# Kernel optimization log

Hardware: AMD Instinct MI355X
Metric: run time of the kernel (lower is better)

Reference implementation:

```python
import jax, jax.numpy as jnp
import numpy as np
from jax import lax

B, C, H, W = 16, 256, 64, 64  # inplanes=256, planes=2*inplanes=512


def ste_sign(x):
    # forward: sign(x); backward: clipped straight-through (|x|<=1)
    c = jnp.clip(x, -1.0, 1.0)
    return c + lax.stop_gradient(jnp.sign(x) - c)


def conv_ada(x, w, ka, kw):
    # 1-bit activations scaled by learnable scalar ka
    a_b = ste_sign(x) * ka
    # 1-bit weights with per-out-channel XNOR-style scale * learnable kw
    alpha = jnp.mean(jnp.abs(w), axis=(1, 2, 3), keepdims=True) * kw  # [O,1,1,1]
    w_b = ste_sign(w) * alpha
    return lax.conv_general_dilated(a_b, w_b, window_strides=(1, 1),
                                    padding=((1, 1), (1, 1)),
                                    dimension_numbers=('NCHW', 'OIHW', 'NCHW'))


def prelu(x, slope):
    s = slope.reshape(1, -1, 1, 1)
    return jnp.where(x >= 0, x, s * x)


def pixel_unshuffle2(x):
    b, c, h, w = x.shape
    x = x.reshape(b, c, h // 2, 2, w // 2, 2)
    x = x.transpose(0, 1, 3, 5, 2, 4)  # (b, c, r1, r2, h2, w2)
    return x.reshape(b, c * 4, h // 2, w // 2)


def setup_inputs() -> dict:
    key = jax.random.key(0)
    ks = jax.random.split(key, 8)
    inp = {
        'x': jax.random.normal(ks[0], (B, C, H, W), dtype=jnp.float32),
        'conv1_w': jax.random.normal(ks[1], (C, C, 3, 3), dtype=jnp.float32) * 0.05,
        'conv2_w': jax.random.normal(ks[2], (C // 2, C, 3, 3), dtype=jnp.float32) * 0.05,
        'bias1_': jnp.zeros((1, C, 1, 1), jnp.float32),
        'bias1': jnp.zeros((1, C, 1, 1), jnp.float32),
        'bias2': jnp.zeros((1, C, 1, 1), jnp.float32),
        'bias2_': jnp.zeros((1, C, 1, 1), jnp.float32),
        'bias3': jnp.zeros((1, C // 2, 1, 1), jnp.float32),
        'bias4': jnp.zeros((1, C // 2, 1, 1), jnp.float32),
        'ka1': jnp.asarray(1.0, jnp.float32),
        'kw1': jnp.asarray(0.2, jnp.float32),
        'ka2': jnp.asarray(1.0, jnp.float32),
        'kw2': jnp.asarray(0.2, jnp.float32),
        'prelu1_w': jnp.full((C,), 0.25, jnp.float32),
        'prelu2_w': jnp.full((C // 2,), 0.25, jnp.float32),
    }
    return inp


def reference(x, conv1_w, conv2_w, bias1_, bias1, bias2, bias2_, bias3, bias4,
              ka1, kw1, ka2, kw2, prelu1_w, prelu2_w):
    out = x + bias1_                      # move1_
    out = conv_ada(out, conv1_w, ka1, kw1)  # conv1
    xres = out + x                        # residual add
    # NOTE: in the original forward, move1/prelu1/move2 output is overwritten
    # (dead branch); kept here for faithfulness but it does not affect output.
    _dead = prelu(out + bias1, prelu1_w) + bias2
    out = xres + bias2_                   # move2_
    out = conv_ada(out, conv2_w, ka2, kw2)  # conv2 -> C//2 channels
    shortcut = xres[:, :xres.shape[1] // 2, :, :]
    out = out + shortcut
    out = out + bias3                     # move3
    out = prelu(out, prelu2_w)            # prelu2
    out = out + bias4                     # move4
    out = pixel_unshuffle2(out)           # -> [B, 2*C, H/2, W/2]
    return out
```

## Files before the change

### kernel.cpp

```cpp
#include <hip/hip_runtime.h>
#include <hip/hip_bf16.h>
#include <stdint.h>

#define B_   16
#define C_   256
#define H_   64
#define W_   64
#define PH   66
#define PW   66
#define K1   2304
#define NO1  256
#define NO2  128

typedef signed char i8;
typedef int   int32x4 __attribute__((ext_vector_type(4)));

__device__ __forceinline__ void gl_lds16(const void* src, void* dst) {
    __builtin_amdgcn_global_load_lds(
        (const __attribute__((address_space(1))) unsigned int*)src,
        (__attribute__((address_space(3))) unsigned int*)dst, 16, 0, 0);
}

__device__ __forceinline__ i8 sign_i8(float v) {
    return (v > 0.f) ? (i8)1 : ((v < 0.f) ? (i8)(-1) : (i8)0);
}

__global__ void halo_zero(i8* __restrict__ s1, i8* __restrict__ s2) {
    int t = blockIdx.x * blockDim.x + threadIdx.x;
    const int total = B_ * PH * PW * (C_ / 16);
    if (t >= total) return;
    int pix = t >> 4;
    int c16 = t & 15;
    int pw  = pix % PW;
    int ph  = (pix / PW) % PH;
    if (ph != 0 && ph != PH - 1 && pw != 0 && pw != PW - 1) return;
    int4 z = make_int4(0, 0, 0, 0);
    *(int4*)(s1 + (size_t)pix * C_ + c16 * 16) = z;
    *(int4*)(s2 + (size_t)pix * C_ + c16 * 16) = z;
}

__global__ void prep_s1(const float* __restrict__ x, const float* __restrict__ bias1_,
                        i8* __restrict__ s1) {
    __shared__ i8 tile[64][272];
    int b = blockIdx.x >> 6;
    int h = blockIdx.x & 63;
    int t = threadIdx.x;
    int w  = t & 63;
    int cq = t >> 6;
    for (int i = 0; i < 64; ++i) {
        int c = cq * 64 + i;
        float v = x[((size_t)(b * C_ + c) * H_ + h) * W_ + w] + bias1_[c];
        tile[w][c] = sign_i8(v);
    }
    __syncthreads();
    for (int i = 0; i < 4; ++i) {
        int idx = i * 256 + t;
        int w2  = idx >> 4;
        int cb  = (idx & 15) * 16;
        int4 v = *(const int4*)&tile[w2][cb];
        *(int4*)(s1 + ((size_t)(b * PH + h + 1) * PW + (w2 + 1)) * C_ + cb) = v;
    }
}

__global__ void prep_w(const float* __restrict__ w1, const float* __restrict__ w2,
                       const float* __restrict__ ka1, const float* __restrict__ kw1,
                       const float* __restrict__ ka2, const float* __restrict__ kw2,
                       i8* __restrict__ Bt1, i8* __restrict__ Bt2,
                       float* __restrict__ scale1, float* __restrict__ scale2) {
    int o = blockIdx.x;
    const float* w; i8* Bt; float* scale; float kk;
    if (o < NO1) { w = w1 + (size_t)o * K1;         Bt = Bt1 + (size_t)o * K1;         scale = scale1 + o;         kk = ka1[0] * kw1[0]; }
    else         { int oo = o - NO1;
                   w = w2 + (size_t)oo * K1;        Bt = Bt2 + (size_t)oo * K1;        scale = scale2 + oo;        kk = ka2[0] * kw2[0]; }
    int t = threadIdx.x;
    float s = 0.f;
    for (int e = t; e < K1; e += 256) {
        float v = w[e];
        s += fabsf(v);
        int c = e / 9, tap = e % 9;
        Bt[tap * 256 + c] = sign_i8(v);
    }
    for (int off = 32; off; off >>= 1) s += __shfl_down(s, off);
    __shared__ float red[4];
    if ((t & 63) == 0) red[t >> 6] = s;
    __syncthreads();
    if (t == 0) {
        float tot = red[0] + red[1] + red[2] + red[3];
        *scale = kk * tot * (1.0f / 2304.0f);
    }
}

template<int EPI>
__global__ __launch_bounds__(512)
void gemm_conv(const i8* __restrict__ Sin, const i8* __restrict__ Bt,
               const float* __restrict__ scale,
               const float* __restrict__ xaux,
               const float* __restrict__ biasA,
               const float* __restrict__ bias4,
               const float* __restrict__ slope,
               i8*   __restrict__ s2out,
               float* __restrict__ xres_out,
               float* __restrict__ dout)
{
    extern __shared__ char lds[];

    int t  = threadIdx.x;

    int wg    = blockIdx.x;
    int chunk = gridDim.x >> 3;
    int logical = (wg & 7) * chunk + (wg >> 3);
    int nb, mb;
    if (EPI == 1) { nb = logical & 1; mb = logical >> 1; }
    else          { nb = 0;           mb = logical; }
    int b  = mb >> 4;
    int h0 = (mb & 15) * 4;

    int r0  = t >> 3;
    int off = ((t & 7) * 16) ^ (((t >> 3) & 7) << 4);
    int lin = (t & 7) * 16;

    int l  = t & 63;
    int wv = t >> 6;
    int wr = wv >> 1;
    int wc = wv & 1;

    int32x4 acc[4][4];
#pragma unroll
    for (int mi = 0; mi < 4; ++mi)
#pragma unroll
        for (int ni = 0; ni < 4; ++ni) acc[mi][ni] = (int32x4){0, 0, 0, 0};

    auto stage = [&](int ks, char* buf) {
        char* As = buf;
        char* Bs = buf + 32768;
        int tap = ks >> 1;
        int c0  = (ks & 1) * 128;
        int dh  = tap / 3, dw = tap % 3;
#pragma unroll
        for (int i = 0; i < 4; ++i) {
            int r  = r0 + i * 64;
            int hh = r >> 6, ww = r & 63;
            const i8* ga = Sin + ((size_t)(b * PH + h0 + hh + dh) * PW + (ww + dw)) * C_ + c0 + off;
            gl_lds16(ga, As + r * 128 + lin);
        }
#pragma unroll
        for (int i = 0; i < 2; ++i) {
            int r = r0 + i * 64;
            int n = nb * 128 + r;
            const i8* gb = Bt + (size_t)n * K1 + tap * 256 + c0 + off;
            gl_lds16(gb, Bs + r * 128 + lin);
        }
    };

    auto compute = [&](const char* buf) {
        const char* As = buf;
        const char* Bs = buf + 32768;
        __builtin_amdgcn_s_setprio(1);
#pragma unroll
        for (int kk = 0; kk < 2; ++kk) {
            int kb = kk * 64 + ((l >> 4) * 16);
            int rx = (l & 7) << 4;
            int32x4 af[4], bf[4];
#pragma unroll
            for (int mi = 0; mi < 4; ++mi)
                af[mi] = *(const int32x4*)(As + (wr * 64 + mi * 16 + (l & 15)) * 128 + (kb ^ rx));
#pragma unroll
            for (int ni = 0; ni < 4; ++ni)
                bf[ni] = *(const int32x4*)(Bs + (wc * 64 + ni * 16 + (l & 15)) * 128 + (kb ^ rx));
#pragma unroll
            for (int mi = 0; mi < 4; ++mi)
#pragma unroll
                for (int ni = 0; ni < 4; ++ni)
                    acc[mi][ni] = __builtin_amdgcn_mfma_i32_16x16x64_i8(af[mi], bf[ni], acc[mi][ni], 0, 0, 0);
        }
        __builtin_amdgcn_s_setprio(0);
    };

    char* bc  = lds;
    char* bn  = lds + 49152;
    char* bn2 = lds + 98304;

    stage(0, bc);
    stage(1, bn);
    asm volatile("s_waitcnt vmcnt(6)" ::: "memory");
    __builtin_amdgcn_s_barrier();

    for (int ks = 0; ks < 18; ++ks) {
        if (ks < 16) stage(ks + 2, bn2);
        compute(bc);
        if (ks < 16)      asm volatile("s_waitcnt vmcnt(6)" ::: "memory");
        else if (ks == 16) asm volatile("s_waitcnt vmcnt(0)" ::: "memory");
        if (ks < 17) __builtin_amdgcn_s_barrier();
        char* tmp = bc; bc = bn; bn = bn2; bn2 = tmp;
    }

    int co = l & 15;
    int ro = l >> 4;
#pragma unroll
    for (int mi = 0; mi < 4; ++mi) {
#pragma unroll
        for (int ni = 0; ni < 4; ++ni) {
            int n_loc = wc * 64 + ni * 16 + co;
            int o = nb * 128 + n_loc;
            float sc = scale[o];
#pragma unroll
            for (int j = 0; j < 4; ++j) {
                int m_loc = wr * 64 + mi * 16 + ro * 4 + j;
                int h = h0 + (m_loc >> 6);
                int w = m_loc & 63;
                float v = (float)acc[mi][ni][j] * sc;
                if (EPI == 1) {
                    float xv = xaux[((size_t)(b * C_ + o) * H_ + h) * W_ + w];
                    float xr = v + xv;
                    float sv = xr + biasA[o];
                    s2out[((size_t)(b * PH + h + 1) * PW + (w + 1)) * C_ + o] = sign_i8(sv);
                    if (o < NO2)
                        xres_out[(((size_t)b * H_ + h) * W_ + w) * NO2 + o] = xr;
                } else {
                    float xr = xaux[(((size_t)b * H_ + h) * W_ + w) * NO2 + o];
                    float vv = v + xr + biasA[o];
                    vv = (vv >= 0.f) ? vv : vv * slope[o];
                    vv += bias4[o];
                    int p = h & 1, q = w & 1;
                    dout[(((size_t)b * 512 + (o * 4 + p * 2 + q)) * 32 + (h >> 1)) * 32 + (w >> 1)] = vv;
                }
            }
        }
    }
}

static const size_t SZ_S   = (size_t)B_ * PH * PW * C_;
static const size_t OFF_S1 = 0;
static const size_t OFF_S2 = OFF_S1 + SZ_S;
static const size_t OFF_B1 = OFF_S2 + SZ_S;
static const size_t OFF_B2 = OFF_B1 + (size_t)NO1 * K1;
static const size_t OFF_C1 = OFF_B2 + (size_t)NO2 * K1;
static const size_t OFF_C2 = OFF_C1 + 1024;
static const size_t OFF_XR = OFF_C2 + 512;

extern "C" void kernel_launch(void* const* d_in, const int* in_sizes, int n_in,
                              void* d_out, int out_size, void* d_ws, size_t ws_size,
                              hipStream_t stream) {
    (void)in_sizes; (void)n_in; (void)out_size; (void)ws_size;
    const float* x      = (const float*)d_in[0];
    const float* w1     = (const float*)d_in[1];
    const float* w2     = (const float*)d_in[2];
    const float* bias1_ = (const float*)d_in[3];
    const float* bias2_ = (const float*)d_in[6];
    const float* bias3  = (const float*)d_in[7];
    const float* bias4  = (const float*)d_in[8];
    const float* ka1    = (const float*)d_in[9];
    const float* kw1    = (const float*)d_in[10];
    const float* ka2    = (const float*)d_in[11];
    const float* kw2    = (const float*)d_in[12];
    const float* slope2 = (const float*)d_in[14];

    char* ws = (char*)d_ws;
    i8*    s1   = (i8*)(ws + OFF_S1);
    i8*    s2   = (i8*)(ws + OFF_S2);
    i8*    Bt1  = (i8*)(ws + OFF_B1);
    i8*    Bt2  = (i8*)(ws + OFF_B2);
    float* sc1  = (float*)(ws + OFF_C1);
    float* sc2  = (float*)(ws + OFF_C2);
    float* xres = (float*)(ws + OFF_XR);
    float* out  = (float*)d_out;

    {
        int total = B_ * PH * PW * (C_ / 16);
        hipLaunchKernelGGL(halo_zero, dim3((total + 255) / 256), dim3(256), 0, stream, s1, s2);
    }
    hipLaunchKernelGGL(prep_s1, dim3(B_ * H_), dim3(256), 0, stream, x, bias1_, s1);
    hipLaunchKernelGGL(prep_w, dim3(NO1 + NO2), dim3(256), 0, stream,
                       w1, w2, ka1, kw1, ka2, kw2, Bt1, Bt2, sc1, sc2);
    hipLaunchKernelGGL((gemm_conv<1>), dim3(512), dim3(512), 147456, stream,
                       s1, Bt1, sc1, x, bias2_, nullptr, nullptr, s2, xres, nullptr);
    hipLaunchKernelGGL((gemm_conv<2>), dim3(256), dim3(512), 147456, stream,
                       s2, Bt2, sc2, xres, bias3, bias4, slope2, nullptr, nullptr, out);
}
```

Measured before the change: 267.6 us.

## Load activation halo tile once into LDS and reuse across all nine taps

```diff
diff --git a/kernel.cpp b/kernel.cpp
--- a/kernel.cpp
+++ b/kernel.cpp
@@ -91,8 +91,9 @@
 }
 
 template<int EPI>
-__global__ __launch_bounds__(512)
-void gemm_conv(const i8* __restrict__ Sin, const i8* __restrict__ Bt,
+__device__ __forceinline__ void conv_body(
+               char* lds,
+               const i8* __restrict__ Sin, const i8* __restrict__ Bt,
                const float* __restrict__ scale,
                const float* __restrict__ xaux,
                const float* __restrict__ biasA,
@@ -102,7 +103,10 @@
                float* __restrict__ xres_out,
                float* __restrict__ dout)
 {
-    extern __shared__ char lds[];
+    char* Alds = lds;
+    char* Bs0  = lds + 101376;
+    char* Bs1  = Bs0 + 16384;
+    char* Bs2  = Bs1 + 16384;
 
     int t  = threadIdx.x;
 
@@ -115,83 +119,99 @@
     int b  = mb >> 4;
     int h0 = (mb & 15) * 4;
 
-    int r0  = t >> 3;
-    int off = ((t & 7) * 16) ^ (((t >> 3) & 7) << 4);
-    int lin = (t & 7) * 16;
-
     int l  = t & 63;
     int wv = t >> 6;
     int wr = wv >> 1;
     int wc = wv & 1;
 
-    int32x4 acc[4][4];
-#pragma unroll
-    for (int mi = 0; mi < 4; ++mi)
-#pragma unroll
-        for (int ni = 0; ni < 4; ++ni) acc[mi][ni] = (int32x4){0, 0, 0, 0};
-
-    auto stage = [&](int ks, char* buf) {
-        char* As = buf;
-        char* Bs = buf + 32768;
+    int br0  = t >> 3;
+    int bsrc = ((t & 7) * 16) ^ (((t >> 3) & 7) << 4);
+    int blin = (t & 7) * 16;
+
+    auto stageB = [&](int ks, char* Bs) {
         int tap = ks >> 1;
         int c0  = (ks & 1) * 128;
-        int dh  = tap / 3, dw = tap % 3;
-#pragma unroll
-        for (int i = 0; i < 4; ++i) {
-            int r  = r0 + i * 64;
-            int hh = r >> 6, ww = r & 63;
-            const i8* ga = Sin + ((size_t)(b * PH + h0 + hh + dh) * PW + (ww + dw)) * C_ + c0 + off;
-            gl_lds16(ga, As + r * 128 + lin);
-        }
 #pragma unroll
         for (int i = 0; i < 2; ++i) {
-            int r = r0 + i * 64;
+            int r = br0 + i * 64;
             int n = nb * 128 + r;
-            const i8* gb = Bt + (size_t)n * K1 + tap * 256 + c0 + off;
-            gl_lds16(gb, Bs + r * 128 + lin);
+            const i8* gb = Bt + (size_t)n * K1 + tap * 256 + c0 + bsrc;
+            gl_lds16(gb, Bs + r * 128 + blin);
         }
     };
 
-    auto compute = [&](const char* buf) {
-        const char* As = buf;
-        const char* Bs = buf + 32768;
-        __builtin_amdgcn_s_setprio(1);
-#pragma unroll
-        for (int kk = 0; kk < 2; ++kk) {
-            int kb = kk * 64 + ((l >> 4) * 16);
-            int rx = (l & 7) << 4;
-            int32x4 af[4], bf[4];
-#pragma unroll
-            for (int mi = 0; mi < 4; ++mi)
-                af[mi] = *(const int32x4*)(As + (wr * 64 + mi * 16 + (l & 15)) * 128 + (kb ^ rx));
-#pragma unroll
-            for (int ni = 0; ni < 4; ++ni)
-                bf[ni] = *(const int32x4*)(Bs + (wc * 64 + ni * 16 + (l & 15)) * 128 + (kb ^ rx));
-#pragma unroll
-            for (int mi = 0; mi < 4; ++mi)
+    stageB(0, Bs0);
+    stageB(1, Bs1);
+    for (int i = 0; i < 13; ++i) {
+        int idx = i * 512 + t;
+        if (idx < 6336) {
+            int r6   = idx / 1056;
+            int rem  = idx - r6 * 1056;
+            int w66  = rem >> 4;
+            int slot = rem & 15;
+            int pix  = r6 * 66 + w66;
+            const i8* ga = Sin + ((size_t)(b * PH + h0 + r6) * PW + w66) * 256
+                               + ((slot ^ (pix & 7)) << 4);
+            gl_lds16(ga, Alds + idx * 16);
+        }
+    }
+    asm volatile("s_waitcnt vmcnt(0)" ::: "memory");
+    __builtin_amdgcn_s_barrier();
+
+    int q = l >> 4;
+    int pixbase[4];
+#pragma unroll
+    for (int mi = 0; mi < 4; ++mi) {
+        int m = wr * 64 + mi * 16 + (l & 15);
+        pixbase[mi] = (m >> 6) * 66 + (m & 63);
+    }
+    int rx = (l & 7) << 4;
+    int bfbase[4];
+#pragma unroll
+    for (int ni = 0; ni < 4; ++ni)
+        bfbase[ni] = (wc * 64 + ni * 16 + (l & 15)) * 128;
+    int bfoff[2] = { (q * 16) ^ rx, (64 + q * 16) ^ rx };
+
+    int32x4 acc[4][4];
+#pragma unroll
+    for (int mi = 0; mi < 4; ++mi)
+#pragma unroll
+        for (int ni = 0; ni < 4; ++ni) acc[mi][ni] = (int32x4){0, 0, 0, 0};
+
+    char* pr = Bs0; char* pn = Bs1; char* ps = Bs2;
+
+    for (int ks = 0; ks < 18; ++ks) {
+        if (ks < 16) stageB(ks + 2, ps);
+        {
+            int tap  = ks >> 1;
+            int toff = (tap / 3) * 66 + (tap % 3);
+            int c8   = (ks & 1) << 7;
+            __builtin_amdgcn_s_setprio(1);
+#pragma unroll
+            for (int kk = 0; kk < 2; ++kk) {
+                int qk = kk * 4 + q;
+                int32x4 af[4], bf[4];
+#pragma unroll
+                for (int mi = 0; mi < 4; ++mi) {
+                    int pixm = pixbase[mi] + toff;
+                    int addr = pixm * 256 + c8 + ((qk ^ (pixm & 7)) << 4);
+                    af[mi] = *(const int32x4*)(Alds + addr);
+                }
 #pragma unroll
                 for (int ni = 0; ni < 4; ++ni)
-                    acc[mi][ni] = __builtin_amdgcn_mfma_i32_16x16x64_i8(af[mi], bf[ni], acc[mi][ni], 0, 0, 0);
+                    bf[ni] = *(const int32x4*)(pr + bfbase[ni] + bfoff[kk]);
+#pragma unroll
+                for (int mi = 0; mi < 4; ++mi)
+#pragma unroll
+                    for (int ni = 0; ni < 4; ++ni)
+                        acc[mi][ni] = __builtin_amdgcn_mfma_i32_16x16x64_i8(af[mi], bf[ni], acc[mi][ni], 0, 0, 0);
+            }
+            __builtin_amdgcn_s_setprio(0);
         }
-        __builtin_amdgcn_s_setprio(0);
-    };
-
-    char* bc  = lds;
-    char* bn  = lds + 49152;
-    char* bn2 = lds + 98304;
-
-    stage(0, bc);
-    stage(1, bn);
-    asm volatile("s_waitcnt vmcnt(6)" ::: "memory");
-    __builtin_amdgcn_s_barrier();
-
-    for (int ks = 0; ks < 18; ++ks) {
-        if (ks < 16) stage(ks + 2, bn2);
-        compute(bc);
-        if (ks < 16)      asm volatile("s_waitcnt vmcnt(6)" ::: "memory");
+        if (ks < 16)      asm volatile("s_waitcnt vmcnt(2)" ::: "memory");
         else if (ks == 16) asm volatile("s_waitcnt vmcnt(0)" ::: "memory");
         if (ks < 17) __builtin_amdgcn_s_barrier();
-        char* tmp = bc; bc = bn; bn = bn2; bn2 = tmp;
+        char* tmp = pr; pr = pn; pn = ps; ps = tmp;
     }
 
     int co = l & 15;
@@ -221,12 +241,27 @@
                     float vv = v + xr + biasA[o];
                     vv = (vv >= 0.f) ? vv : vv * slope[o];
                     vv += bias4[o];
-                    int p = h & 1, q = w & 1;
-                    dout[(((size_t)b * 512 + (o * 4 + p * 2 + q)) * 32 + (h >> 1)) * 32 + (w >> 1)] = vv;
+                    int p = h & 1, qq = w & 1;
+                    dout[(((size_t)b * 512 + (o * 4 + p * 2 + qq)) * 32 + (h >> 1)) * 32 + (w >> 1)] = vv;
                 }
             }
         }
     }
+}
+
+__global__ __launch_bounds__(512) void conv_g1(
+    const i8* Sin, const i8* Bt, const float* scale, const float* xaux,
+    const float* biasA, const float* bias4, const float* slope,
+    i8* s2out, float* xres_out, float* dout) {
+    extern __shared__ char lds[];
+    conv_body<1>(lds, Sin, Bt, scale, xaux, biasA, bias4, slope, s2out, xres_out, dout);
+}
+__global__ __launch_bounds__(512) void conv_g2(
+    const i8* Sin, const i8* Bt, const float* scale, const float* xaux,
+    const float* biasA, const float* bias4, const float* slope,
+    i8* s2out, float* xres_out, float* dout) {
+    extern __shared__ char lds[];
+    conv_body<2>(lds, Sin, Bt, scale, xaux, biasA, bias4, slope, s2out, xres_out, dout);
 }
 
 static const size_t SZ_S   = (size_t)B_ * PH * PW * C_;
@@ -237,6 +272,8 @@
 static const size_t OFF_C1 = OFF_B2 + (size_t)NO2 * K1;
 static const size_t OFF_C2 = OFF_C1 + 1024;
 static const size_t OFF_XR = OFF_C2 + 512;
+
+static const int LDS_BYTES = 101376 + 3 * 16384;
 
 extern "C" void kernel_launch(void* const* d_in, const int* in_sizes, int n_in,
                               void* d_out, int out_size, void* d_ws, size_t ws_size,
@@ -272,8 +309,8 @@
     hipLaunchKernelGGL(prep_s1, dim3(B_ * H_), dim3(256), 0, stream, x, bias1_, s1);
     hipLaunchKernelGGL(prep_w, dim3(NO1 + NO2), dim3(256), 0, stream,
                        w1, w2, ka1, kw1, ka2, kw2, Bt1, Bt2, sc1, sc2);
-    hipLaunchKernelGGL((gemm_conv<1>), dim3(512), dim3(512), 147456, stream,
+    hipLaunchKernelGGL(conv_g1, dim3(512), dim3(512), LDS_BYTES, stream,
                        s1, Bt1, sc1, x, bias2_, nullptr, nullptr, s2, xres, nullptr);
-    hipLaunchKernelGGL((gemm_conv<2>), dim3(256), dim3(512), 147456, stream,
+    hipLaunchKernelGGL(conv_g2, dim3(256), dim3(512), LDS_BYTES, stream,
                        s2, Bt2, sc2, xres, bias3, bias4, slope2, nullptr, nullptr, out);
 }
```

Measured after the change: 266.8 us. Within noise of the previous version (-0.3%).
